# Kernel tuning notes

Hardware: AMD Instinct MI355X
Metric: run time of the kernel (lower is better)

Reference implementation:

```python
import jax, jax.numpy as jnp
import numpy as np
import math

IN_DIM = 768
FREQ = IN_DIM // 2 + 1          # 385
K = max(1, int(FREQ * 0.1))     # 38
MLP_IN = 2 * K                  # 76
HID = 256
LN_EPS = 1e-5


def _spectral_mask(task_id=0):
    # Faithful port of PiNoiseBiLoRA._get_spectral_mask
    avail = np.arange(1, FREQ)
    mt = 20
    idx = avail[task_id % mt::mt]
    if len(idx) >= K:
        idx = idx[:K]
    else:
        needed = K - len(idx)
        rf = math.ceil(needed / len(idx))
        idx = np.concatenate([idx, np.tile(idx, rf)[:needed]])
    return idx.astype(np.int32)


def setup_inputs() -> dict:
    key = jax.random.key(0)
    ks = jax.random.split(key, 6)
    B, S = 8, 4096
    x = jax.random.normal(ks[0], (B, S, IN_DIM), dtype=jnp.float32)
    eps = jax.random.normal(ks[1], (B, S, MLP_IN), dtype=jnp.float32)
    indices = jnp.asarray(_spectral_mask(0))
    w_scale = 0.05
    mu_w1 = jax.random.normal(ks[2], (HID, MLP_IN), dtype=jnp.float32) * w_scale
    mu_w2 = jax.random.normal(ks[3], (MLP_IN, HID), dtype=jnp.float32) * w_scale
    sg_w1 = jax.random.normal(ks[4], (HID, MLP_IN), dtype=jnp.float32) * w_scale
    sg_w2 = jax.random.normal(ks[5], (MLP_IN, HID), dtype=jnp.float32) * w_scale
    zeros_h = jnp.zeros((HID,), jnp.float32)
    zeros_o = jnp.zeros((MLP_IN,), jnp.float32)
    ones_h = jnp.ones((HID,), jnp.float32)
    return {
        'x': x, 'eps': eps, 'indices': indices,
        'mu_w1': mu_w1, 'mu_b1': zeros_h, 'mu_g': ones_h, 'mu_beta': zeros_h,
        'mu_w2': mu_w2, 'mu_b2': zeros_o,
        'sg_w1': sg_w1, 'sg_b1': zeros_h, 'sg_g': ones_h, 'sg_beta': zeros_h,
        'sg_w2': sg_w2, 'sg_b2': zeros_o,
    }


def _mlp(x, w1, b1, g, beta, w2, b2):
    # Linear -> LayerNorm -> GELU(exact) -> Linear
    h = x @ w1.T + b1
    mu = h.mean(axis=-1, keepdims=True)
    var = jnp.mean((h - mu) ** 2, axis=-1, keepdims=True)
    h = (h - mu) * jax.lax.rsqrt(var + LN_EPS) * g + beta
    h = jax.nn.gelu(h, approximate=False)
    return h @ w2.T + b2


def reference(x, eps, indices,
              mu_w1, mu_b1, mu_g, mu_beta, mu_w2, mu_b2,
              sg_w1, sg_b1, sg_g, sg_beta, sg_w2, sg_b2):
    # Training-mode forward of PiNoiseBiLoRA
    x_freq = jnp.fft.rfft(x, axis=-1)            # [B,S,FREQ] complex64
    x_sel = x_freq[..., indices]                 # gather k freq bins
    x_in = jnp.concatenate([x_sel.real, x_sel.imag], axis=-1)  # [B,S,2k]
    mu = _mlp(x_in, mu_w1, mu_b1, mu_g, mu_beta, mu_w2, mu_b2)
    sigma = _mlp(x_in, sg_w1, sg_b1, sg_g, sg_beta, sg_w2, sg_b2)
    z = mu + eps * sigma                         # reparameterization
    z_complex = jax.lax.complex(z[..., :K], z[..., K:]).astype(jnp.complex64)
    noise = jnp.zeros(x_freq.shape, jnp.complex64).at[..., indices].add(z_complex)
    return jnp.fft.irfft(noise, n=IN_DIM, axis=-1)
```

## Files before the change

kernel.cpp:

```cpp
#include <hip/hip_runtime.h>
#include <hip/hip_bf16.h>
#include <math.h>

#define INDIM 768
#define NROWS 32768
#define KSEL  38
#define NCOLS 76
#define HID   256
#define LN_EPS 1e-5f

typedef float  f32x4  __attribute__((ext_vector_type(4)));
typedef __bf16 bf16x8 __attribute__((ext_vector_type(8)));

#define MFMA16(a,b,c) __builtin_amdgcn_mfma_f32_16x16x32_bf16((a),(b),(c),0,0,0)

#define OFF_BFP 0
#define OFF_W1P 122880
#define OFF_W2P 221184
#define OFF_BSP 303104
#define OFF_Z1  450560
#define OFF_Z2  6742016

__global__ void k_prep(const int* __restrict__ idxs,
                       const float* __restrict__ mu_w1, const float* __restrict__ sg_w1,
                       const float* __restrict__ mu_w2, const float* __restrict__ sg_w2,
                       __bf16* __restrict__ BfP, __bf16* __restrict__ W1P,
                       __bf16* __restrict__ W2P, __bf16* __restrict__ BsP)
{
    int tid = blockIdx.x * blockDim.x + threadIdx.x;
    int nth = gridDim.x * blockDim.x;
    const float TH = 6.28318530717958647692f / (float)INDIM;

    for (int e = tid; e < 120 * 512; e += nth) {
        int frag = e >> 9, lane = (e >> 3) & 63, j = e & 7;
        int kc = frag / 5, nt = frag % 5;
        int c = nt * 16 + (lane & 15);
        int k = kc * 32 + ((lane >> 4) << 3) + j;
        float v = 0.f;
        if (c < NCOLS) {
            int cc = (c < KSEL) ? c : c - KSEL;
            int f = idxs[cc];
            int m = (f * k) % INDIM;
            float s, co; sincosf(TH * (float)m, &s, &co);
            v = (c < KSEL) ? co : -s;
        }
        BfP[e] = (__bf16)v;
    }
    for (int e = tid; e < 96 * 512; e += nth) {
        int frag = e >> 9, lane = (e >> 3) & 63, j = e & 7;
        int mlp = frag / 48; int r = frag % 48;
        int nt = r / 3, ks = r % 3;
        int row = nt * 16 + (lane & 15);
        int k = ks * 32 + ((lane >> 4) << 3) + j;
        const float* W = mlp ? sg_w1 : mu_w1;
        W1P[e] = (__bf16)((k < NCOLS) ? W[row * NCOLS + k] : 0.f);
    }
    for (int e = tid; e < 80 * 512; e += nth) {
        int frag = e >> 9, lane = (e >> 3) & 63, j = e & 7;
        int mlp = frag / 40; int r = frag % 40;
        int nt = r / 8, ks = r % 8;
        int row = nt * 16 + (lane & 15);
        int k = ks * 32 + ((lane >> 4) << 3) + j;
        const float* W = mlp ? sg_w2 : mu_w2;
        W2P[e] = (__bf16)((row < NCOLS) ? W[row * HID + k] : 0.f);
    }
    for (int e = tid; e < 144 * 512; e += nth) {
        int frag = e >> 9, lane = (e >> 3) & 63, j = e & 7;
        int nt = frag / 3, ks = frag % 3;
        int n = nt * 16 + (lane & 15);
        int k = ks * 32 + ((lane >> 4) << 3) + j;
        float v = 0.f;
        if (k < NCOLS) {
            int cc = (k < KSEL) ? k : k - KSEL;
            int f = idxs[cc];
            int m = (f * n) % INDIM;
            float s, co; sincosf(TH * (float)m, &s, &co);
            v = ((k < KSEL) ? co : -s) * (2.0f / (float)INDIM);
        }
        BsP[e] = (__bf16)v;
    }
}

static __device__ inline float gelu_fast(float v) {
    float u = v * (0.79788456080286535588f + 0.03567740813636141f * v * v);
    return v / (1.f + __expf(-2.f * u));
}

__global__ __launch_bounds__(256, 8) void k_dft(
    const float* __restrict__ x, const __bf16* __restrict__ Bf,
    __bf16* __restrict__ z1)
{
    __shared__ __align__(16) float PA[3][1280];
    int tid = threadIdx.x;
    int w = tid >> 6, lane = tid & 63, q = lane >> 4, l16 = lane & 15;
    int rbase = blockIdx.x * 16;

    f32x4 acc[5] = {};
    const float* xrow = x + (size_t)(rbase + l16) * INDIM + w * 192 + q * 8;
    const __bf16* bfb = Bf + (size_t)(w * 30) * 512 + (size_t)lane * 8;
    #pragma unroll
    for (int kk = 0; kk < 6; ++kk) {
        float4 f0 = ((const float4*)(xrow + kk * 32))[0];
        float4 f1 = ((const float4*)(xrow + kk * 32))[1];
        union { __bf16 h[8]; bf16x8 v; } a;
        a.h[0]=(__bf16)f0.x; a.h[1]=(__bf16)f0.y; a.h[2]=(__bf16)f0.z; a.h[3]=(__bf16)f0.w;
        a.h[4]=(__bf16)f1.x; a.h[5]=(__bf16)f1.y; a.h[6]=(__bf16)f1.z; a.h[7]=(__bf16)f1.w;
        #pragma unroll
        for (int nt = 0; nt < 5; ++nt) {
            bf16x8 b = *(const bf16x8*)(bfb + (size_t)(kk * 5 + nt) * 512);
            acc[nt] = MFMA16(a.v, b, acc[nt]);
        }
    }
    if (w > 0) {
        #pragma unroll
        for (int nt = 0; nt < 5; ++nt)
            #pragma unroll
            for (int r = 0; r < 4; ++r)
                PA[w - 1][(q * 4 + r) * 80 + nt * 16 + l16] = acc[nt][r];
    }
    __syncthreads();
    if (w == 0) {
        #pragma unroll
        for (int nt = 0; nt < 5; ++nt)
            #pragma unroll
            for (int r = 0; r < 4; ++r) {
                int i = (q * 4 + r) * 80 + nt * 16 + l16;
                float v = acc[nt][r] + PA[0][i] + PA[1][i] + PA[2][i];
                z1[(size_t)(rbase + q * 4 + r) * 96 + nt * 16 + l16] = (__bf16)v;
            }
        #pragma unroll
        for (int r = 0; r < 4; ++r)
            ((unsigned short*)z1)[(size_t)(rbase + q * 4 + r) * 96 + 80 + l16] = 0;
    }
}

__global__ __launch_bounds__(256, 4) void k_mlp(
    const __bf16* __restrict__ z1, const float* __restrict__ eps,
    const __bf16* __restrict__ W1f, const __bf16* __restrict__ W2f,
    const float* __restrict__ mu_b1, const float* __restrict__ mu_g,
    const float* __restrict__ mu_be, const float* __restrict__ mu_b2,
    const float* __restrict__ sg_b1, const float* __restrict__ sg_g,
    const float* __restrict__ sg_be, const float* __restrict__ sg_b2,
    __bf16* __restrict__ z2)
{
    __shared__ __align__(16) float  PA[2][1280];
    __shared__ __align__(16) __bf16 GW[4][2176];
    int tid = threadIdx.x;
    int w = tid >> 6, lane = tid & 63, q = lane >> 4, l16 = lane & 15;
    int t = w >> 1, p = w & 1;
    int rbase = blockIdx.x * 32 + t * 16;

    bf16x8 a1[3];
    #pragma unroll
    for (int ks = 0; ks < 3; ++ks)
        a1[ks] = *(const bf16x8*)(z1 + (size_t)(rbase + l16) * 96 + ks * 32 + q * 8);

    const float* b1 = p ? sg_b1 : mu_b1;
    const float* g  = p ? sg_g  : mu_g;
    const float* be = p ? sg_be : mu_be;

    const __bf16* w1b = W1f + (size_t)(p * 48) * 512 + (size_t)lane * 8;
    f32x4 h[16] = {};
    #pragma unroll
    for (int nt = 0; nt < 16; ++nt)
        #pragma unroll
        for (int ks = 0; ks < 3; ++ks) {
            bf16x8 b = *(const bf16x8*)(w1b + (size_t)(nt * 3 + ks) * 512);
            h[nt] = MFMA16(a1[ks], b, h[nt]);
        }
    float s[4] = {}, ss[4] = {};
    #pragma unroll
    for (int nt = 0; nt < 16; ++nt) {
        float bb = b1[nt * 16 + l16];
        #pragma unroll
        for (int r = 0; r < 4; ++r) {
            float v = h[nt][r] + bb; h[nt][r] = v;
            s[r] += v; ss[r] += v * v;
        }
    }
    #pragma unroll
    for (int off = 1; off < 16; off <<= 1)
        #pragma unroll
        for (int r = 0; r < 4; ++r) {
            s[r] += __shfl_xor(s[r], off); ss[r] += __shfl_xor(ss[r], off);
        }
    float mean[4], rstd[4];
    #pragma unroll
    for (int r = 0; r < 4; ++r) {
        mean[r] = s[r] * (1.f / 256.f);
        rstd[r] = rsqrtf(ss[r] * (1.f / 256.f) - mean[r] * mean[r] + LN_EPS);
    }
    __bf16* gw = &GW[w][0];
    bf16x8 a2[8];
    #pragma unroll
    for (int half = 0; half < 2; ++half) {
        #pragma unroll
        for (int ntl = 0; ntl < 8; ++ntl) {
            int nt = half * 8 + ntl;
            int i = nt * 16 + l16;
            float gv = g[i], bev = be[i];
            #pragma unroll
            for (int r = 0; r < 4; ++r)
                gw[(q * 4 + r) * 136 + ntl * 16 + l16] =
                    (__bf16)gelu_fast((h[nt][r] - mean[r]) * rstd[r] * gv + bev);
        }
        #pragma unroll
        for (int ks = 0; ks < 4; ++ks)
            a2[half * 4 + ks] = *(const bf16x8*)&gw[l16 * 136 + ks * 32 + q * 8];
    }
    const __bf16* w2b = W2f + (size_t)(p * 40) * 512 + (size_t)lane * 8;
    f32x4 o[5] = {};
    #pragma unroll
    for (int nt = 0; nt < 5; ++nt)
        #pragma unroll
        for (int ks = 0; ks < 8; ++ks) {
            bf16x8 b = *(const bf16x8*)(w2b + (size_t)(nt * 8 + ks) * 512);
            o[nt] = MFMA16(a2[ks], b, o[nt]);
        }
    float ev[5][4];
    if (p == 0) {
        #pragma unroll
        for (int nt = 0; nt < 5; ++nt)
            #pragma unroll
            for (int r = 0; r < 4; ++r)
                PA[t][(q * 4 + r) * 80 + nt * 16 + l16] = o[nt][r];
    } else {
        #pragma unroll
        for (int nt = 0; nt < 5; ++nt) {
            int j = nt * 16 + l16;
            #pragma unroll
            for (int r = 0; r < 4; ++r)
                ev[nt][r] = (j < NCOLS)
                    ? eps[(size_t)(rbase + q * 4 + r) * NCOLS + j] : 0.f;
        }
    }
    __syncthreads();
    if (p == 1) {
        #pragma unroll
        for (int nt = 0; nt < 5; ++nt) {
            int j = nt * 16 + l16;
            float b2m = (j < NCOLS) ? mu_b2[j] : 0.f;
            float b2s = (j < NCOLS) ? sg_b2[j] : 0.f;
            #pragma unroll
            for (int r = 0; r < 4; ++r) {
                float z = 0.f;
                if (j < NCOLS) {
                    float omu = PA[t][(q * 4 + r) * 80 + j];
                    z = (omu + b2m) + ev[nt][r] * (o[nt][r] + b2s);
                }
                z2[(size_t)(rbase + q * 4 + r) * 96 + j] = (__bf16)z;
            }
        }
        #pragma unroll
        for (int r = 0; r < 4; ++r)
            ((unsigned short*)z2)[(size_t)(rbase + q * 4 + r) * 96 + 80 + l16] = 0;
    }
}

__global__ __launch_bounds__(256, 8) void k_syn(
    const __bf16* __restrict__ z2, const __bf16* __restrict__ Bs,
    float* __restrict__ out)
{
    int tid = threadIdx.x;
    int w = tid >> 6, lane = tid & 63, q = lane >> 4, l16 = lane & 15;
    int rbase = blockIdx.x * 16;

    bf16x8 az[3];
    #pragma unroll
    for (int ks = 0; ks < 3; ++ks)
        az[ks] = *(const bf16x8*)(z2 + (size_t)(rbase + l16) * 96 + ks * 32 + q * 8);

    const __bf16* bsb = Bs + (size_t)(w * 36) * 512 + (size_t)lane * 8;
    #pragma unroll 4
    for (int ntl = 0; ntl < 12; ++ntl) {
        f32x4 oc = {};
        #pragma unroll
        for (int ks = 0; ks < 3; ++ks) {
            bf16x8 b = *(const bf16x8*)(bsb + (size_t)(ntl * 3 + ks) * 512);
            oc = MFMA16(az[ks], b, oc);
        }
        #pragma unroll
        for (int r = 0; r < 4; ++r)
            out[(size_t)(rbase + q * 4 + r) * INDIM + w * 192 + ntl * 16 + l16] = oc[r];
    }
}

extern "C" void kernel_launch(void* const* d_in, const int* in_sizes, int n_in,
                              void* d_out, int out_size, void* d_ws, size_t ws_size,
                              hipStream_t stream)
{
    const float* x     = (const float*)d_in[0];
    const float* eps   = (const float*)d_in[1];
    const int*   idxs  = (const int*)  d_in[2];
    const float* mu_w1 = (const float*)d_in[3];
    const float* mu_b1 = (const float*)d_in[4];
    const float* mu_g  = (const float*)d_in[5];
    const float* mu_be = (const float*)d_in[6];
    const float* mu_w2 = (const float*)d_in[7];
    const float* mu_b2 = (const float*)d_in[8];
    const float* sg_w1 = (const float*)d_in[9];
    const float* sg_b1 = (const float*)d_in[10];
    const float* sg_g  = (const float*)d_in[11];
    const float* sg_be = (const float*)d_in[12];
    const float* sg_w2 = (const float*)d_in[13];
    const float* sg_b2 = (const float*)d_in[14];
    float* out = (float*)d_out;

    char* ws = (char*)d_ws;
    __bf16* BfP = (__bf16*)(ws + OFF_BFP);
    __bf16* W1P = (__bf16*)(ws + OFF_W1P);
    __bf16* W2P = (__bf16*)(ws + OFF_W2P);
    __bf16* BsP = (__bf16*)(ws + OFF_BSP);
    __bf16* Z1  = (__bf16*)(ws + OFF_Z1);
    __bf16* Z2  = (__bf16*)(ws + OFF_Z2);

    hipLaunchKernelGGL(k_prep, dim3(1024), dim3(256), 0, stream,
                       idxs, mu_w1, sg_w1, mu_w2, sg_w2, BfP, W1P, W2P, BsP);
    hipLaunchKernelGGL(k_dft, dim3(NROWS / 16), dim3(256), 0, stream,
                       x, BfP, Z1);
    hipLaunchKernelGGL(k_mlp, dim3(NROWS / 32), dim3(256), 0, stream,
                       Z1, eps, W1P, W2P,
                       mu_b1, mu_g, mu_be, mu_b2,
                       sg_b1, sg_g, sg_be, sg_b2, Z2);
    hipLaunchKernelGGL(k_syn, dim3(NROWS / 16), dim3(256), 0, stream,
                       Z2, BsP, out);
}
```

Baseline: 252.7 us.

## Stage DFT and synthesis operands through LDS with double-buffered async global loads

k_dft now processes 64 rows per 512-thread block. It streams x and the DFT basis through double-buffered shared memory using global_load_lds, with XOR swizzling to avoid bank conflicts. The basis is widened to 96 columns so two wave groups split the output columns, which removes the cross-wave LDS reduction. k_syn likewise stages the synthesis basis through double-buffered LDS shared by 4 row tiles, so basis data is reused instead of being re-read from global per wave. The cost is more block-wide barriers per k-step and larger LDS use, which may limit occupancy.

```diff
diff --git a/kernel.cpp b/kernel.cpp
--- a/kernel.cpp
+++ b/kernel.cpp
@@ -15,11 +15,11 @@
 #define MFMA16(a,b,c) __builtin_amdgcn_mfma_f32_16x16x32_bf16((a),(b),(c),0,0,0)
 
 #define OFF_BFP 0
-#define OFF_W1P 122880
-#define OFF_W2P 221184
-#define OFF_BSP 303104
-#define OFF_Z1  450560
-#define OFF_Z2  6742016
+#define OFF_W1P 147456
+#define OFF_W2P 245760
+#define OFF_BSP 327680
+#define OFF_Z1  475136
+#define OFF_Z2  6766592
 
 __global__ void k_prep(const int* __restrict__ idxs,
                        const float* __restrict__ mu_w1, const float* __restrict__ sg_w1,
@@ -31,9 +31,9 @@
     int nth = gridDim.x * blockDim.x;
     const float TH = 6.28318530717958647692f / (float)INDIM;
 
-    for (int e = tid; e < 120 * 512; e += nth) {
+    for (int e = tid; e < 144 * 512; e += nth) {
         int frag = e >> 9, lane = (e >> 3) & 63, j = e & 7;
-        int kc = frag / 5, nt = frag % 5;
+        int kc = frag / 6, nt = frag % 6;
         int c = nt * 16 + (lane & 15);
         int k = kc * 32 + ((lane >> 4) << 3) + j;
         float v = 0.f;
@@ -86,52 +86,66 @@
     return v / (1.f + __expf(-2.f * u));
 }
 
-__global__ __launch_bounds__(256, 8) void k_dft(
+typedef __attribute__((address_space(1))) const unsigned int g_u32;
+typedef __attribute__((address_space(3))) unsigned int l_u32;
+
+__global__ __launch_bounds__(512, 8) void k_dft(
     const float* __restrict__ x, const __bf16* __restrict__ Bf,
     __bf16* __restrict__ z1)
 {
-    __shared__ __align__(16) float PA[3][1280];
+    __shared__ __align__(16) char R[28672];
     int tid = threadIdx.x;
     int w = tid >> 6, lane = tid & 63, q = lane >> 4, l16 = lane & 15;
-    int rbase = blockIdx.x * 16;
-
-    f32x4 acc[5] = {};
-    const float* xrow = x + (size_t)(rbase + l16) * INDIM + w * 192 + q * 8;
-    const __bf16* bfb = Bf + (size_t)(w * 30) * 512 + (size_t)lane * 8;
-    #pragma unroll
-    for (int kk = 0; kk < 6; ++kk) {
-        float4 f0 = ((const float4*)(xrow + kk * 32))[0];
-        float4 f1 = ((const float4*)(xrow + kk * 32))[1];
+    int t = w >> 1, g = w & 1;
+    int rbase = blockIdx.x * 64;
+
+    int xrow_u = (lane >> 3);
+    int xcol_f = ((lane & 7) ^ xrow_u) << 2;
+
+    f32x4 acc[3] = {};
+    {
+        const float* sx = x + (size_t)(rbase + w * 8 + xrow_u) * INDIM + xcol_f;
+        __builtin_amdgcn_global_load_lds((g_u32*)sx, (l_u32*)(R + w * 1024), 16, 0, 0);
+        if (w < 6)
+            __builtin_amdgcn_global_load_lds(
+                (g_u32*)(Bf + (size_t)w * 512 + lane * 8),
+                (l_u32*)(R + 16384 + w * 1024), 16, 0, 0);
+    }
+    __syncthreads();
+
+    for (int kk = 0; kk < 24; ++kk) {
+        int buf = kk & 1;
+        if (kk < 23) {
+            const float* sx = x + (size_t)(rbase + w * 8 + xrow_u) * INDIM
+                                + (kk + 1) * 32 + xcol_f;
+            __builtin_amdgcn_global_load_lds((g_u32*)sx,
+                (l_u32*)(R + (buf ^ 1) * 8192 + w * 1024), 16, 0, 0);
+            if (w < 6)
+                __builtin_amdgcn_global_load_lds(
+                    (g_u32*)(Bf + (size_t)((kk + 1) * 6 + w) * 512 + lane * 8),
+                    (l_u32*)(R + 16384 + (buf ^ 1) * 6144 + w * 1024), 16, 0, 0);
+        }
+        const char* xb = R + buf * 8192 + (t * 16 + l16) * 128;
+        int s = (l16 & 7) << 4;
+        f32x4 f0 = *(const f32x4*)(xb + ((q * 32) ^ s));
+        f32x4 f1 = *(const f32x4*)(xb + (((q * 32) + 16) ^ s));
         union { __bf16 h[8]; bf16x8 v; } a;
-        a.h[0]=(__bf16)f0.x; a.h[1]=(__bf16)f0.y; a.h[2]=(__bf16)f0.z; a.h[3]=(__bf16)f0.w;
-        a.h[4]=(__bf16)f1.x; a.h[5]=(__bf16)f1.y; a.h[6]=(__bf16)f1.z; a.h[7]=(__bf16)f1.w;
-        #pragma unroll
-        for (int nt = 0; nt < 5; ++nt) {
-            bf16x8 b = *(const bf16x8*)(bfb + (size_t)(kk * 5 + nt) * 512);
-            acc[nt] = MFMA16(a.v, b, acc[nt]);
-        }
-    }
-    if (w > 0) {
-        #pragma unroll
-        for (int nt = 0; nt < 5; ++nt)
-            #pragma unroll
-            for (int r = 0; r < 4; ++r)
-                PA[w - 1][(q * 4 + r) * 80 + nt * 16 + l16] = acc[nt][r];
-    }
-    __syncthreads();
-    if (w == 0) {
-        #pragma unroll
-        for (int nt = 0; nt < 5; ++nt)
-            #pragma unroll
-            for (int r = 0; r < 4; ++r) {
-                int i = (q * 4 + r) * 80 + nt * 16 + l16;
-                float v = acc[nt][r] + PA[0][i] + PA[1][i] + PA[2][i];
-                z1[(size_t)(rbase + q * 4 + r) * 96 + nt * 16 + l16] = (__bf16)v;
-            }
+        a.h[0]=(__bf16)f0[0]; a.h[1]=(__bf16)f0[1]; a.h[2]=(__bf16)f0[2]; a.h[3]=(__bf16)f0[3];
+        a.h[4]=(__bf16)f1[0]; a.h[5]=(__bf16)f1[1]; a.h[6]=(__bf16)f1[2]; a.h[7]=(__bf16)f1[3];
+        const char* bb = R + 16384 + buf * 6144 + g * 3072 + (size_t)lane * 16;
+        #pragma unroll
+        for (int ntl = 0; ntl < 3; ++ntl) {
+            bf16x8 b = *(const bf16x8*)(bb + ntl * 1024);
+            acc[ntl] = MFMA16(a.v, b, acc[ntl]);
+        }
+        __syncthreads();
+    }
+    #pragma unroll
+    for (int ntl = 0; ntl < 3; ++ntl)
         #pragma unroll
         for (int r = 0; r < 4; ++r)
-            ((unsigned short*)z1)[(size_t)(rbase + q * 4 + r) * 96 + 80 + l16] = 0;
-    }
+            z1[(size_t)(rbase + t * 16 + q * 4 + r) * 96 + g * 48 + ntl * 16 + l16]
+                = (__bf16)acc[ntl][r];
 }
 
 __global__ __launch_bounds__(256, 4) void k_mlp(
@@ -257,32 +271,55 @@
     }
 }
 
-__global__ __launch_bounds__(256, 8) void k_syn(
+__global__ __launch_bounds__(512, 8) void k_syn(
     const __bf16* __restrict__ z2, const __bf16* __restrict__ Bs,
     float* __restrict__ out)
 {
+    __shared__ __align__(16) char R[49152];
     int tid = threadIdx.x;
     int w = tid >> 6, lane = tid & 63, q = lane >> 4, l16 = lane & 15;
-    int rbase = blockIdx.x * 16;
+    int t = w >> 1, g = w & 1;
+    int rbase = blockIdx.x * 64;
 
     bf16x8 az[3];
     #pragma unroll
     for (int ks = 0; ks < 3; ++ks)
-        az[ks] = *(const bf16x8*)(z2 + (size_t)(rbase + l16) * 96 + ks * 32 + q * 8);
-
-    const __bf16* bsb = Bs + (size_t)(w * 36) * 512 + (size_t)lane * 8;
-    #pragma unroll 4
-    for (int ntl = 0; ntl < 12; ++ntl) {
-        f32x4 oc = {};
-        #pragma unroll
-        for (int ks = 0; ks < 3; ++ks) {
-            bf16x8 b = *(const bf16x8*)(bsb + (size_t)(ntl * 3 + ks) * 512);
-            oc = MFMA16(az[ks], b, oc);
-        }
-        #pragma unroll
-        for (int r = 0; r < 4; ++r)
-            out[(size_t)(rbase + q * 4 + r) * INDIM + w * 192 + ntl * 16 + l16] = oc[r];
-    }
+        az[ks] = *(const bf16x8*)(z2 + (size_t)(rbase + t * 16 + l16) * 96
+                                     + ks * 32 + q * 8);
+
+    #define SYN_STAGE(c, dst)                                                  \
+        _Pragma("unroll")                                                      \
+        for (int uu = 0; uu < 3; ++uu) {                                       \
+            int u = w + uu * 8;                                                \
+            int frag = (u < 12) ? (12 * (c) + u) : (72 + 12 * (c) + (u - 12)); \
+            __builtin_amdgcn_global_load_lds(                                  \
+                (g_u32*)(Bs + (size_t)frag * 512 + lane * 8),                  \
+                (l_u32*)((dst) + u * 1024), 16, 0, 0);                         \
+        }
+
+    SYN_STAGE(0, R)
+    __syncthreads();
+    for (int c = 0; c < 6; ++c) {
+        int buf = c & 1;
+        if (c < 5) SYN_STAGE(c + 1, R + (buf ^ 1) * 24576)
+        const char* bb = R + buf * 24576 + g * 12288 + (size_t)lane * 16;
+        #pragma unroll
+        for (int ntl = 0; ntl < 4; ++ntl) {
+            f32x4 oc = {};
+            #pragma unroll
+            for (int ks = 0; ks < 3; ++ks) {
+                bf16x8 b = *(const bf16x8*)(bb + (ntl * 3 + ks) * 1024);
+                oc = MFMA16(az[ks], b, oc);
+            }
+            int nt = g * 24 + 4 * c + ntl;
+            #pragma unroll
+            for (int r = 0; r < 4; ++r)
+                out[(size_t)(rbase + t * 16 + q * 4 + r) * INDIM + nt * 16 + l16]
+                    = oc[r];
+        }
+        if (c < 5) __syncthreads();
+    }
+    #undef SYN_STAGE
 }
 
 extern "C" void kernel_launch(void* const* d_in, const int* in_sizes, int n_in,
@@ -316,12 +353,12 @@
 
     hipLaunchKernelGGL(k_prep, dim3(1024), dim3(256), 0, stream,
                        idxs, mu_w1, sg_w1, mu_w2, sg_w2, BfP, W1P, W2P, BsP);
-    hipLaunchKernelGGL(k_dft, dim3(NROWS / 16), dim3(256), 0, stream,
+    hipLaunchKernelGGL(k_dft, dim3(NROWS / 64), dim3(512), 0, stream,
                        x, BfP, Z1);
     hipLaunchKernelGGL(k_mlp, dim3(NROWS / 32), dim3(256), 0, stream,
                        Z1, eps, W1P, W2P,
                        mu_b1, mu_g, mu_be, mu_b2,
                        sg_b1, sg_g, sg_be, sg_b2, Z2);
-    hipLaunchKernelGGL(k_syn, dim3(NROWS / 16), dim3(256), 0, stream,
+    hipLaunchKernelGGL(k_syn, dim3(NROWS / 64), dim3(512), 0, stream,
                        Z2, BsP, out);
 }
```

Measured after the change: 248.5 us. Within noise of the previous version (-1.7%).
